# Optimization experiments

Hardware: AMD Instinct MI355X
Metric: run time of the kernel (lower is better)

The kernel has to match this reference:

```python
import jax, jax.numpy as jnp
import numpy as np

N_NODES = 100      # fixed: actor_fc expects 6000 = 100 * 60
IN_C    = 65536    # chev_conv_state_dim
OUT_C   = 60
K       = 3        # Chebyshev order
ACTION  = 100
N_EDGES = 1600


def setup_inputs() -> dict:
    key = jax.random.key(0)
    ks = jax.random.split(key, 20)
    s = 0.02  # small init scale
    f32 = jnp.float32
    return {
        "substrate_features": jax.random.normal(ks[0], (N_NODES, IN_C), f32),
        "substrate_edge_index": jax.random.randint(ks[1], (2, N_EDGES), 0, N_NODES),
        "vnr_features": jax.random.uniform(ks[2], (1, 3), f32),
        # ChebConv params: weight [K, IN_C, OUT_C], bias [OUT_C]
        "actor_cheb_w": (jax.random.normal(ks[3], (K, IN_C, OUT_C), f32) * s),
        "actor_cheb_b": jnp.zeros((OUT_C,), f32),
        "critic_cheb_w": (jax.random.normal(ks[4], (K, IN_C, OUT_C), f32) * s),
        "critic_cheb_b": jnp.zeros((OUT_C,), f32),
        # three Linear(1,60) per head, stacked: w [3, 60], b [3, 60]
        "actor_vnr_w": jax.random.normal(ks[5], (3, OUT_C), f32) * s,
        "actor_vnr_b": jnp.zeros((3, OUT_C), f32),
        "critic_vnr_w": jax.random.normal(ks[6], (3, OUT_C), f32) * s,
        "critic_vnr_b": jnp.zeros((3, OUT_C), f32),
        # heads
        "actor_fc_w": jax.random.normal(ks[7], (N_NODES * OUT_C, ACTION), f32) * s,
        "actor_fc_b": jnp.zeros((ACTION,), f32),
        "critic_fc_w": jax.random.normal(ks[8], (N_NODES * OUT_C, 1), f32) * s,
        "critic_fc_b": jnp.zeros((1,), f32),
    }


def _cheb_conv(x, src, dst, W, b):
    """PyG ChebConv with sym normalization, lambda_max=2 => L_hat = -D^-1/2 A D^-1/2.
    Z0 = x, Z1 = L_hat x, Z2 = 2 L_hat Z1 - Z0; out = sum_k Zk @ W[k] + b."""
    n = x.shape[0]
    ones = jnp.ones(src.shape[0], x.dtype)
    deg = jax.ops.segment_sum(ones, src, num_segments=n)
    dinv = jnp.where(deg > 0, jax.lax.rsqrt(jnp.maximum(deg, 1.0)), 0.0)
    w_norm = -dinv[src] * dinv[dst]  # [E]

    def lhat(z):  # sparse propagate: gather src rows, scale, scatter-add at dst
        return jax.ops.segment_sum(w_norm[:, None] * z[src], dst, num_segments=n)

    z0 = x
    z1 = lhat(z0)
    z2 = 2.0 * lhat(z1) - z0
    return z0 @ W[0] + z1 @ W[1] + z2 @ W[2] + b


def _vnr_sum(v, w, b):
    # sum of three Linear(1,60) outputs on scalars v[0], v[1], v[2] -> [60]
    return (v[:, None] * w + b).sum(axis=0)


def reference(substrate_features, substrate_edge_index, vnr_features,
              actor_cheb_w, actor_cheb_b, critic_cheb_w, critic_cheb_b,
              actor_vnr_w, actor_vnr_b, critic_vnr_w, critic_vnr_b,
              actor_fc_w, actor_fc_b, critic_fc_w, critic_fc_b):
    src, dst = substrate_edge_index[0], substrate_edge_index[1]
    v = vnr_features[0]  # [3]

    emb_a = jnp.tanh(_cheb_conv(substrate_features, src, dst, actor_cheb_w, actor_cheb_b))
    emb_a = emb_a + _vnr_sum(v, actor_vnr_w, actor_vnr_b)  # broadcast [N,60] + [60]
    flat_a = emb_a.reshape(1, -1)  # [1, 6000]
    logits = flat_a @ actor_fc_w + actor_fc_b  # [1, ACTION]

    emb_c = jnp.tanh(_cheb_conv(substrate_features, src, dst, critic_cheb_w, critic_cheb_b))
    emb_c = emb_c + _vnr_sum(v, critic_vnr_w, critic_vnr_b)
    flat_c = emb_c.reshape(1, -1)
    values = flat_c @ critic_fc_w + critic_fc_b  # [1, 1]

    return logits, values
```

## Files before the change

kernel.cpp:

```cpp
#include <hip/hip_runtime.h>
#include <math.h>

#define KDIM    65536
#define NNODES  100
#define OUTC    60
#define YW      64
#define YSLAB   (NNODES*YW)

#define BK3     256
#define NKC3    (KDIM/BK3)
#define CHUNK   256
#define NKC     256
#define STEPS   (CHUNK/32)

#define WS_S    0
#define WS_Y    10048
#define WS_E    48448
#define XB_OFF_BYTES   245760ull
#define XB_BYTES       (100ull*65536ull*2ull)
#define WS_NEED_BYTES  (XB_OFF_BYTES + XB_BYTES)

typedef short bf16x8 __attribute__((ext_vector_type(8)));
typedef float f32x4  __attribute__((ext_vector_type(4)));
typedef unsigned short ushort8 __attribute__((ext_vector_type(8)));

__device__ inline unsigned short f2bf(float f) {
    union { float f; unsigned u; } x; x.f = f;
    unsigned r = x.u + 0x7FFFu + ((x.u >> 16) & 1u);
    return (unsigned short)(r >> 16);
}

__global__ __launch_bounds__(256) void k_build_s(const int* __restrict__ ei,
                                                 float* __restrict__ S) {
    __shared__ int   deg[NNODES];
    __shared__ float dinv[NNODES];
    const int t = threadIdx.x;
    if (t < NNODES) deg[t] = 0;
    __syncthreads();
    const int* src = ei;
    const int* dst = ei + 1600;
    for (int e = t; e < 1600; e += 256) atomicAdd(&deg[src[e]], 1);
    __syncthreads();
    if (t < NNODES) { int d = deg[t]; dinv[t] = (d > 0) ? rsqrtf((float)d) : 0.f; }
    __syncthreads();
    for (int e = t; e < 1600; e += 256) {
        int s = src[e], d = dst[e];
        atomicAdd(&S[d * NNODES + s], -dinv[s] * dinv[d]);
    }
}

__global__ __launch_bounds__(256) void k_cvt_x(const float* __restrict__ x,
                                               ushort8* __restrict__ xb) {
    int g = blockIdx.x * 256 + threadIdx.x;
    for (int i = g; i < 819200; i += 204800) {
        const float4 lo = ((const float4*)x)[2 * i];
        const float4 hi = ((const float4*)x)[2 * i + 1];
        ushort8 o;
        o[0] = f2bf(lo.x); o[1] = f2bf(lo.y); o[2] = f2bf(lo.z); o[3] = f2bf(lo.w);
        o[4] = f2bf(hi.x); o[5] = f2bf(hi.y); o[6] = f2bf(hi.z); o[7] = f2bf(hi.w);
        xb[i] = o;
    }
}

__global__ __launch_bounds__(512, 4) void k_gemm3(const unsigned short* __restrict__ xb,
                                                  const float* __restrict__ wa,
                                                  const float* __restrict__ wc,
                                                  float* __restrict__ Y) {
    __shared__ float Wl[BK3 * OUTC];
    const int hk   = blockIdx.x;
    const int kc   = blockIdx.y;
    const int wave = threadIdx.x >> 6;
    const int lane = threadIdx.x & 63;
    const int nt   = wave & 3;
    const int mh   = wave >> 2;
    const int n16  = lane & 15;
    const int quad = lane >> 4;
    const int NT   = mh ? 3 : 4;
    const int c0   = nt * 16;
    const int cidx = min(c0 + n16, OUTC - 1);

    const float* Wg = (hk < 3 ? wa : wc)
                    + (size_t)(hk % 3) * ((size_t)KDIM * OUTC)
                    + (size_t)kc * (BK3 * OUTC);
    for (int i = wave; i < 60; i += 8) {
        const float* gp = Wg + i * 256 + lane * 4;
        __builtin_amdgcn_global_load_lds(
            (const __attribute__((address_space(1))) void*)gp,
            (__attribute__((address_space(3))) void*)&Wl[i * 256], 16, 0, 0);
    }

    const unsigned short* ap[4];
#pragma unroll
    for (int t = 0; t < 4; ++t)
        ap[t] = xb + (size_t)min(n16 + 16 * (mh * 4 + t), NNODES - 1) * KDIM
                   + kc * BK3 + quad * 8;

    __syncthreads();

    f32x4 acc[4] = {};
#pragma unroll
    for (int s = 0; s < BK3 / 32; ++s) {
        bf16x8 bfr;
#pragma unroll
        for (int j = 0; j < 8; ++j) {
            int jj = (j + quad * 2) & 7;
            bfr[jj] = (short)f2bf(Wl[(s * 32 + quad * 8 + jj) * OUTC + cidx]);
        }
#pragma unroll
        for (int t = 0; t < 4; ++t) {
            if (t < NT) {
                bf16x8 afr = *(const bf16x8*)(ap[t] + s * 32);
                acc[t] = __builtin_amdgcn_mfma_f32_16x16x32_bf16(afr, bfr, acc[t], 0, 0, 0);
            }
        }
    }

    float* Yb = Y + hk * YSLAB;
#pragma unroll
    for (int t = 0; t < 4; ++t) {
        if (t < NT) {
#pragma unroll
            for (int r = 0; r < 4; ++r) {
                int row = (mh * 4 + t) * 16 + quad * 4 + r;
                if (row < NNODES)
                    atomicAdd(&Yb[row * YW + c0 + n16], acc[t][r]);
            }
        }
    }
}

__global__ __launch_bounds__(256, 2) void k_gemm_f32(const float* __restrict__ x,
                                                     const float* __restrict__ wa,
                                                     const float* __restrict__ wc,
                                                     float* __restrict__ Y) {
    const int hk   = blockIdx.x;
    const int kc   = blockIdx.y;
    const int wave = threadIdx.x >> 6;
    const int lane = threadIdx.x & 63;
    const int n16  = lane & 15;
    const int quad = lane >> 4;
    const float* W = (hk < 3 ? wa : wc) + (size_t)(hk % 3) * ((size_t)KDIM * OUTC);
    const int c0   = wave * 16;
    const int cidx = min(c0 + n16, OUTC - 1);
    const int kb0  = kc * CHUNK + quad * 8;
    const float* ap[7];
#pragma unroll
    for (int t = 0; t < 7; ++t)
        ap[t] = x + (size_t)min(n16 + 16 * t, NNODES - 1) * KDIM + kb0;
    const float* bp = W + (size_t)kb0 * OUTC + cidx;
    f32x4 acc[7] = {};
#pragma unroll 2
    for (int s = 0; s < STEPS; ++s) {
        bf16x8 bfr;
        const float* q = bp + (size_t)s * 32 * OUTC;
#pragma unroll
        for (int j = 0; j < 8; ++j) bfr[j] = (short)f2bf(q[j * OUTC]);
#pragma unroll
        for (int t = 0; t < 7; ++t) {
            const float* p = ap[t] + s * 32;
            float4 lo = *(const float4*)p;
            float4 hi = *(const float4*)(p + 4);
            bf16x8 afr;
            afr[0] = (short)f2bf(lo.x); afr[1] = (short)f2bf(lo.y);
            afr[2] = (short)f2bf(lo.z); afr[3] = (short)f2bf(lo.w);
            afr[4] = (short)f2bf(hi.x); afr[5] = (short)f2bf(hi.y);
            afr[6] = (short)f2bf(hi.z); afr[7] = (short)f2bf(hi.w);
            acc[t] = __builtin_amdgcn_mfma_f32_16x16x32_bf16(afr, bfr, acc[t], 0, 0, 0);
        }
    }
    float* Yb = Y + hk * YSLAB;
#pragma unroll
    for (int t = 0; t < 7; ++t)
#pragma unroll
        for (int r = 0; r < 4; ++r) {
            int row = t * 16 + quad * 4 + r;
            if (row < NNODES)
                atomicAdd(&Yb[row * YW + c0 + n16], acc[t][r]);
        }
}

__global__ __launch_bounds__(128) void k_emb(const float* __restrict__ S,
                                             const float* __restrict__ Y,
                                             const float* __restrict__ vnr,
                                             const float* __restrict__ avw,
                                             const float* __restrict__ avb,
                                             const float* __restrict__ cvw,
                                             const float* __restrict__ cvb,
                                             const float* __restrict__ acb,
                                             const float* __restrict__ ccb,
                                             const float* __restrict__ afcb,
                                             const float* __restrict__ cfcb,
                                             float* __restrict__ E,
                                             float* __restrict__ out) {
    __shared__ float Sp[NNODES * 101];
    __shared__ float y0[NNODES], y1[NNODES], y2[NNODES], t2[NNODES];
    const int b = blockIdx.x, head = b / OUTC, c = b % OUTC;
    const int t = threadIdx.x;

    for (int i = t; i < NNODES * NNODES; i += 128)
        Sp[(i / NNODES) * 101 + (i % NNODES)] = S[i];
    const float* Yh = Y + (size_t)head * 3 * YSLAB;
    if (t < NNODES) {
        y0[t] = Yh[t * YW + c];
        y1[t] = Yh[YSLAB + t * YW + c];
        y2[t] = Yh[2 * YSLAB + t * YW + c];
    }
    if (b == 0 && t < 101) out[t] = (t < 100) ? afcb[t] : cfcb[0];
    __syncthreads();

    float z1 = 0.f, s2 = 0.f;
    if (t < NNODES) {
        const float* sr = Sp + t * 101;
        for (int m = 0; m < NNODES; ++m) { z1 += sr[m] * y1[m]; s2 += sr[m] * y2[m]; }
        t2[t] = s2;
    }
    __syncthreads();
    if (t < NNODES) {
        const float* sr = Sp + t * 101;
        float t3 = 0.f;
        for (int m = 0; m < NNODES; ++m) t3 += sr[m] * t2[m];
        const float* cb = head ? ccb : acb;
        const float* vw = head ? cvw : avw;
        const float* vb = head ? cvb : avb;
        float u  = y0[t] + z1 + 2.f * t3 - y2[t] + cb[c];
        float vs = vnr[0] * vw[c]        + vb[c]
                 + vnr[1] * vw[OUTC + c] + vb[OUTC + c]
                 + vnr[2] * vw[2*OUTC+c] + vb[2*OUTC+c];
        E[head * (NNODES * OUTC) + t * OUTC + c] = tanhf(u) + vs;
    }
}

__global__ __launch_bounds__(128) void k_heads(const float* __restrict__ E,
                                               const float* __restrict__ afw,
                                               const float* __restrict__ cfw,
                                               float* __restrict__ out) {
    __shared__ float ea[25], ec[25];
    const int b = blockIdx.x, t = threadIdx.x;
    const int f0 = b * 25;
    if (t < 25) {
        ea[t] = E[f0 + t];
        ec[t] = E[NNODES * OUTC + f0 + t];
    }
    __syncthreads();
    if (t < 100) {
        float s = 0.f;
#pragma unroll
        for (int i = 0; i < 25; ++i) s += ea[i] * afw[(size_t)(f0 + i) * 100 + t];
        atomicAdd(&out[t], s);
    } else if (t == 100) {
        float s = 0.f;
#pragma unroll
        for (int i = 0; i < 25; ++i) s += ec[i] * cfw[f0 + i];
        atomicAdd(&out[100], s);
    }
}

extern "C" void kernel_launch(void* const* d_in, const int* in_sizes, int n_in,
                              void* d_out, int out_size, void* d_ws, size_t ws_size,
                              hipStream_t stream) {
    const float* x    = (const float*)d_in[0];
    const int*   ei   = (const int*)  d_in[1];
    const float* vnr  = (const float*)d_in[2];
    const float* wa   = (const float*)d_in[3];
    const float* acb  = (const float*)d_in[4];
    const float* wc   = (const float*)d_in[5];
    const float* ccb  = (const float*)d_in[6];
    const float* avw  = (const float*)d_in[7];
    const float* avb  = (const float*)d_in[8];
    const float* cvw  = (const float*)d_in[9];
    const float* cvb  = (const float*)d_in[10];
    const float* afw  = (const float*)d_in[11];
    const float* afcb = (const float*)d_in[12];
    const float* cfw  = (const float*)d_in[13];
    const float* cfcb = (const float*)d_in[14];

    float* ws = (float*)d_ws;
    float* S  = ws + WS_S;
    float* Y  = ws + WS_Y;
    float* E  = ws + WS_E;
    float* out = (float*)d_out;

    hipMemsetAsync(ws, 0, (size_t)WS_E * sizeof(float), stream);
    k_build_s<<<1, 256, 0, stream>>>(ei, S);

    if (ws_size >= WS_NEED_BYTES) {
        unsigned short* xb = (unsigned short*)((char*)d_ws + XB_OFF_BYTES);
        k_cvt_x<<<800, 256, 0, stream>>>(x, (ushort8*)xb);
        k_gemm3<<<dim3(6, NKC3), 512, 0, stream>>>(xb, wa, wc, Y);
    } else {
        k_gemm_f32<<<dim3(6, NKC), 256, 0, stream>>>(x, wa, wc, Y);
    }

    k_emb<<<120, 128, 0, stream>>>(S, Y, vnr, avw, avb, cvw, cvb,
                                   acb, ccb, afcb, cfcb, E, out);
    k_heads<<<240, 128, 0, stream>>>(E, afw, cfw, out);
}
```

Measured before the change: 238.1 us.

## Double-buffer A and W tiles in LDS with async DMA in split-K GEMM

Replaces the single-shot GEMM kernel with one where each block walks a 512-wide K slab in 64-wide steps. The next step's bf16 activation rows and f32 weight tile are loaded into a second LDS buffer through global_load_lds while the current step computes. Activations are staged in LDS with an XOR swizzle instead of being read straight from global memory. Each wave now covers all 7 row tiles for its 16 columns, so there are half as many blocks and half as many atomic flushes, at the cost of more LDS and fewer blocks to fill the machine.

```diff
diff --git a/kernel.cpp b/kernel.cpp
--- a/kernel.cpp
+++ b/kernel.cpp
@@ -7,8 +7,10 @@
 #define YW      64
 #define YSLAB   (NNODES*YW)
 
-#define BK3     256
-#define NKC3    (KDIM/BK3)
+#define BK5     64
+#define ITERS5  8
+#define SLAB5   (BK5*ITERS5)
+#define NKC5    (KDIM/SLAB5)
 #define CHUNK   256
 #define NKC     256
 #define STEPS   (CHUNK/32)
@@ -62,54 +64,63 @@
     }
 }
 
-__global__ __launch_bounds__(512, 4) void k_gemm3(const unsigned short* __restrict__ xb,
-                                                  const float* __restrict__ wa,
-                                                  const float* __restrict__ wc,
-                                                  float* __restrict__ Y) {
-    __shared__ float Wl[BK3 * OUTC];
+__global__ __launch_bounds__(256) void k_gemm5(const unsigned short* __restrict__ xb,
+                                               const float* __restrict__ wa,
+                                               const float* __restrict__ wc,
+                                               float* __restrict__ Y) {
+    __shared__ unsigned short Ab[2][112 * BK5];
+    __shared__ float          Wf[2][BK5 * OUTC];
     const int hk   = blockIdx.x;
     const int kc   = blockIdx.y;
     const int wave = threadIdx.x >> 6;
     const int lane = threadIdx.x & 63;
-    const int nt   = wave & 3;
-    const int mh   = wave >> 2;
     const int n16  = lane & 15;
     const int quad = lane >> 4;
-    const int NT   = mh ? 3 : 4;
-    const int c0   = nt * 16;
+    const int c0   = wave * 16;
     const int cidx = min(c0 + n16, OUTC - 1);
-
-    const float* Wg = (hk < 3 ? wa : wc)
-                    + (size_t)(hk % 3) * ((size_t)KDIM * OUTC)
-                    + (size_t)kc * (BK3 * OUTC);
-    for (int i = wave; i < 60; i += 8) {
-        const float* gp = Wg + i * 256 + lane * 4;
-        __builtin_amdgcn_global_load_lds(
-            (const __attribute__((address_space(1))) void*)gp,
-            (__attribute__((address_space(3))) void*)&Wl[i * 256], 16, 0, 0);
-    }
-
-    const unsigned short* ap[4];
-#pragma unroll
-    for (int t = 0; t < 4; ++t)
-        ap[t] = xb + (size_t)min(n16 + 16 * (mh * 4 + t), NNODES - 1) * KDIM
-                   + kc * BK3 + quad * 8;
-
-    __syncthreads();
-
-    f32x4 acc[4] = {};
-#pragma unroll
-    for (int s = 0; s < BK3 / 32; ++s) {
-        bf16x8 bfr;
-#pragma unroll
-        for (int j = 0; j < 8; ++j) {
-            int jj = (j + quad * 2) & 7;
-            bfr[jj] = (short)f2bf(Wl[(s * 32 + quad * 8 + jj) * OUTC + cidx]);
-        }
-#pragma unroll
-        for (int t = 0; t < 4; ++t) {
-            if (t < NT) {
-                bf16x8 afr = *(const bf16x8*)(ap[t] + s * 32);
+    const int kb0  = kc * SLAB5;
+
+    const float* Wg = (hk < 3 ? wa : wc) + (size_t)(hk % 3) * ((size_t)KDIM * OUTC);
+
+    auto DMA = [&](int buf, int kb) {
+        for (int j = wave; j < 14; j += 4) {
+            int chunk = j * 64 + lane;
+            int m  = chunk >> 3;
+            int cc = (chunk & 7) ^ (m & 7);
+            const unsigned short* src = xb + (size_t)min(m, NNODES - 1) * KDIM + kb + cc * 8;
+            __builtin_amdgcn_global_load_lds(
+                (const __attribute__((address_space(1))) void*)src,
+                (__attribute__((address_space(3))) void*)&Ab[buf][j * 512], 16, 0, 0);
+        }
+        const float* wsrc = Wg + (size_t)kb * OUTC;
+        for (int j = wave; j < 15; j += 4) {
+            __builtin_amdgcn_global_load_lds(
+                (const __attribute__((address_space(1))) void*)(wsrc + j * 256 + lane * 4),
+                (__attribute__((address_space(3))) void*)&Wf[buf][j * 256], 16, 0, 0);
+        }
+    };
+
+    DMA(0, kb0);
+    f32x4 acc[7] = {};
+
+#pragma unroll
+    for (int it = 0; it < ITERS5; ++it) {
+        __syncthreads();
+        if (it + 1 < ITERS5) DMA((it + 1) & 1, kb0 + (it + 1) * BK5);
+        const unsigned short* A = Ab[it & 1];
+        const float*          B = Wf[it & 1];
+#pragma unroll
+        for (int s = 0; s < 2; ++s) {
+            bf16x8 bfr;
+#pragma unroll
+            for (int j = 0; j < 8; ++j) {
+                int jj = (j + quad * 2) & 7;
+                bfr[jj] = (short)f2bf(B[(s * 32 + quad * 8 + jj) * OUTC + cidx]);
+            }
+            int ch = (s * 4 + quad) ^ (n16 & 7);
+#pragma unroll
+            for (int t = 0; t < 7; ++t) {
+                bf16x8 afr = *(const bf16x8*)(A + (t * 16 + n16) * BK5 + ch * 8);
                 acc[t] = __builtin_amdgcn_mfma_f32_16x16x32_bf16(afr, bfr, acc[t], 0, 0, 0);
             }
         }
@@ -117,16 +128,13 @@
 
     float* Yb = Y + hk * YSLAB;
 #pragma unroll
-    for (int t = 0; t < 4; ++t) {
-        if (t < NT) {
-#pragma unroll
-            for (int r = 0; r < 4; ++r) {
-                int row = (mh * 4 + t) * 16 + quad * 4 + r;
-                if (row < NNODES)
-                    atomicAdd(&Yb[row * YW + c0 + n16], acc[t][r]);
-            }
-        }
-    }
+    for (int t = 0; t < 7; ++t)
+#pragma unroll
+        for (int r = 0; r < 4; ++r) {
+            int row = t * 16 + quad * 4 + r;
+            if (row < NNODES)
+                atomicAdd(&Yb[row * YW + c0 + n16], acc[t][r]);
+        }
 }
 
 __global__ __launch_bounds__(256, 2) void k_gemm_f32(const float* __restrict__ x,
@@ -286,7 +294,7 @@
     if (ws_size >= WS_NEED_BYTES) {
         unsigned short* xb = (unsigned short*)((char*)d_ws + XB_OFF_BYTES);
         k_cvt_x<<<800, 256, 0, stream>>>(x, (ushort8*)xb);
-        k_gemm3<<<dim3(6, NKC3), 512, 0, stream>>>(xb, wa, wc, Y);
+        k_gemm5<<<dim3(6, NKC5), 256, 0, stream>>>(xb, wa, wc, Y);
     } else {
         k_gemm_f32<<<dim3(6, NKC), 256, 0, stream>>>(x, wa, wc, Y);
     }
```

New measurement: 214.2 us. 1.11x faster.
